# Performance work log

Hardware: AMD Instinct MI355X
Metric: run time of the kernel (lower is better)

## Reference

```python
import jax, jax.numpy as jnp
import numpy as np

HEADS = 12
IDX = 0


def setup_inputs() -> dict:
    key = jax.random.key(0)
    ks = jax.random.split(key, 6)
    B, H, W, C = 16, 64, 64, 384
    x = jax.random.normal(ks[0], (B, H * W, C), dtype=jnp.float32)
    qkv_w = jax.random.normal(ks[1], (3 * C, C), dtype=jnp.float32) * 0.02
    proj_w = jax.random.normal(ks[2], (C, C), dtype=jnp.float32) * 0.02
    proj_b = jax.random.normal(ks[3], (C,), dtype=jnp.float32) * 0.02
    lepe_w = jax.random.normal(ks[4], (C, 1, 3, 3), dtype=jnp.float32) * 0.02  # depthwise, torch OIHW with I=1
    lepe_b = jax.random.normal(ks[5], (C,), dtype=jnp.float32) * 0.02
    return {"x": x, "qkv_w": qkv_w, "proj_w": proj_w, "proj_b": proj_b,
            "lepe_w": lepe_w, "lepe_b": lepe_b, "H": H, "W": W}


def _lepe_forward(x, qkv_w, proj_w, proj_b, lepe_w, lepe_b, H, W):
    B, N, C = x.shape
    hd = C // HEADS
    scale = hd ** (-0.5)
    x_img = x.reshape(B, H, W, C)

    if IDX == 0:
        # vertical strips: attend over H within each column
        x_split = jnp.transpose(x_img, (0, 2, 1, 3)).reshape(B * W, H, C)
    else:
        x_split = x_img.reshape(B * H, W, C)
    S, L, _ = x_split.shape

    qkv = (x_split @ qkv_w.T).reshape(S, L, 3, HEADS, hd)
    qkv = jnp.transpose(qkv, (2, 0, 3, 1, 4))  # (3, S, heads, L, hd)
    q, k, v = qkv[0], qkv[1], qkv[2]

    attn = jnp.einsum('shld,shmd->shlm', q, k) * scale
    attn = jax.nn.softmax(attn, axis=-1)
    out = jnp.einsum('shlm,shmd->shld', attn, v)           # (S, heads, L, hd)
    out = jnp.transpose(out, (0, 2, 1, 3)).reshape(S, L, C)
    # faithful to torch: view(B, out_H, out_W, C).view(B, H*W, C) -- no permute back for idx==0
    out_flat = out.reshape(B, H * W, C)

    # depthwise 3x3 conv LePE on the original (H, W) layout
    lepe = jax.lax.conv_general_dilated(
        jnp.transpose(x_img, (0, 3, 1, 2)), lepe_w,
        window_strides=(1, 1), padding='SAME',
        feature_group_count=C,
        dimension_numbers=('NCHW', 'OIHW', 'NCHW'))
    lepe = lepe + lepe_b[None, :, None, None]
    lepe = jnp.transpose(lepe, (0, 2, 3, 1)).reshape(B, H * W, C)

    return (out_flat + lepe) @ proj_w.T + proj_b


def reference(x, qkv_w, proj_w, proj_b, lepe_w, lepe_b, H, W):
    return _lepe_forward(x, qkv_w, proj_w, proj_b, lepe_w, lepe_b, H, W)
```

## Files before the change

### kernel.cpp

```cpp
#include <hip/hip_runtime.h>


typedef _Float16 f16;
typedef _Float16 f16x8 __attribute__((ext_vector_type(8)));
typedef float    f32x4 __attribute__((ext_vector_type(4)));

__device__ __forceinline__ f32x4 mfma_16x16x32(f16x8 a, f16x8 b, f32x4 c) {
  return __builtin_amdgcn_mfma_f32_16x16x32_f16(a, b, c, 0, 0, 0);
}

__global__ __launch_bounds__(256) void k_cvt(const float* __restrict__ src,
                                             f16* __restrict__ dst, int n8) {
  int i = blockIdx.x * 256 + threadIdx.x;
  if (i >= n8) return;
  const f32x4* s4 = (const f32x4*)src;
  f32x4 a = s4[2 * i], b = s4[2 * i + 1];
  f16x8 o;
#pragma unroll
  for (int j = 0; j < 4; ++j) { o[j] = (f16)a[j]; o[4 + j] = (f16)b[j]; }
  *(f16x8*)&dst[(long)i * 8] = o;
}

template <int NDIM, bool FINAL>
__global__ __launch_bounds__(256) void k_gemm(const f16* __restrict__ A,
                                              const f16* __restrict__ Bt,
                                              const float* __restrict__ bias,
                                              f16* __restrict__ Ch,
                                              float* __restrict__ Cf) {
  constexpr int KD = 384;
  constexpr int LDSP = 72;
  constexpr int NT = NDIM / 128;
  __shared__ f16 As[128 * LDSP];
  __shared__ f16 Bs[128 * LDSP];

  const int tid = threadIdx.x;
  const int lane = tid & 63;
  const int wave = tid >> 6;
  const int wr = wave >> 1, wc = wave & 1;
  const int ln = lane & 15, quad = lane >> 4;
  const int q8 = quad * 8;
  const int mt = blockIdx.x / NT;
  const int nt = blockIdx.x % NT;
  const long m0 = (long)mt * 128;
  const int n0 = nt * 128;

  f32x4 acc[4][4] = {};

  for (int k0 = 0; k0 < KD; k0 += 64) {
#pragma unroll
    for (int r = 0; r < 4; ++r) {
      int flat = r * 256 + tid;
      int row = flat >> 3;
      int kk = (flat & 7) * 8;
      f16x8 av = *(const f16x8*)&A[(m0 + row) * KD + k0 + kk];
      *(f16x8*)&As[row * LDSP + kk] = av;
      f16x8 bv = *(const f16x8*)&Bt[(long)(n0 + row) * KD + k0 + kk];
      *(f16x8*)&Bs[row * LDSP + kk] = bv;
    }
    __syncthreads();
#pragma unroll
    for (int ks = 0; ks < 2; ++ks) {
      f16x8 a[4], b[4];
#pragma unroll
      for (int i = 0; i < 4; ++i)
        a[i] = *(const f16x8*)&As[(wr * 64 + i * 16 + ln) * LDSP + ks * 32 + q8];
#pragma unroll
      for (int j = 0; j < 4; ++j)
        b[j] = *(const f16x8*)&Bs[(wc * 64 + j * 16 + ln) * LDSP + ks * 32 + q8];
#pragma unroll
      for (int i = 0; i < 4; ++i)
#pragma unroll
        for (int j = 0; j < 4; ++j)
          acc[i][j] = mfma_16x16x32(a[i], b[j], acc[i][j]);
    }
    __syncthreads();
  }

#pragma unroll
  for (int i = 0; i < 4; ++i) {
#pragma unroll
    for (int j = 0; j < 4; ++j) {
      int gc = n0 + wc * 64 + j * 16 + ln;
#pragma unroll
      for (int r = 0; r < 4; ++r) {
        long gr = m0 + wr * 64 + i * 16 + quad * 4 + r;
        float v = acc[i][j][r];
        if (FINAL)
          Cf[gr * NDIM + gc] = v + bias[gc];
        else
          Ch[gr * (long)NDIM + gc] = (f16)v;
      }
    }
  }
}

__global__ __launch_bounds__(256) void k_lepe(const f16* __restrict__ x16,
                                              const float* __restrict__ lw,
                                              const float* __restrict__ lb,
                                              f16* __restrict__ afused) {
  __shared__ float ws[384 * 9];
  __shared__ float bs[384];
  for (int i = threadIdx.x; i < 384 * 9; i += 256) ws[i] = lw[i];
  for (int i = threadIdx.x; i < 384; i += 256) bs[i] = lb[i];
  __syncthreads();

  int chunk = blockIdx.x * 256 + threadIdx.x;
  int token = chunk / 48;
  int c0 = (chunk % 48) * 8;
  int b = token >> 12, n = token & 4095;
  int h = n >> 6, w = n & 63;

  float acc[8];
#pragma unroll
  for (int cc = 0; cc < 8; ++cc) acc[cc] = bs[c0 + cc];
#pragma unroll
  for (int ky = 0; ky < 3; ++ky) {
    int hh = h + ky - 1;
    if (hh < 0 || hh > 63) continue;
#pragma unroll
    for (int kx = 0; kx < 3; ++kx) {
      int ww = w + kx - 1;
      if (ww < 0 || ww > 63) continue;
      f16x8 xv = *(const f16x8*)&x16[((long)((b << 12) + (hh << 6) + ww)) * 384 + c0];
#pragma unroll
      for (int cc = 0; cc < 8; ++cc)
        acc[cc] += (float)xv[cc] * ws[(c0 + cc) * 9 + ky * 3 + kx];
    }
  }
  f16x8 o;
#pragma unroll
  for (int cc = 0; cc < 8; ++cc) o[cc] = (f16)acc[cc];
  *(f16x8*)&afused[(long)token * 384 + c0] = o;
}

__global__ __launch_bounds__(64) void k_attn(const f16* __restrict__ qkv,
                                             f16* __restrict__ afused) {
  __shared__ f16 vt[32 * 72];
  __shared__ f16 qkbuf[2 * 64 * 56];
  f16* qs = qkbuf;
  f16* ks = qkbuf + 64 * 56;
  f16* ps = qkbuf;

  const int lane = threadIdx.x;
  const int hh = blockIdx.x % 12;
  const int s = blockIdx.x / 12;
  const int b = s >> 6, w = s & 63;
  const int ln = lane & 15, quad = lane >> 4;
  const int q8 = quad * 8;
  const long baseTok = ((long)b << 12) + w;

#pragma unroll
  for (int r = 0; r < 4; ++r) {
    int flat = r * 64 + lane;
    int l = flat >> 2;
    int dg = (flat & 3) * 8;
    long ta = (baseTok + (long)l * 64) * 1152 + hh * 32 + dg;
    f16x8 qv = *(const f16x8*)&qkv[ta];
    f16x8 kv = *(const f16x8*)&qkv[ta + 384];
    f16x8 vv = *(const f16x8*)&qkv[ta + 768];
    *(f16x8*)&qs[l * 56 + dg] = qv;
    *(f16x8*)&ks[l * 56 + dg] = kv;
#pragma unroll
    for (int ii = 0; ii < 8; ++ii) vt[(dg + ii) * 72 + l] = vv[ii];
  }
  __syncthreads();

  f16x8 aq[4], bk[4];
#pragma unroll
  for (int i = 0; i < 4; ++i) aq[i] = *(const f16x8*)&qs[(i * 16 + ln) * 56 + q8];
#pragma unroll
  for (int j = 0; j < 4; ++j) bk[j] = *(const f16x8*)&ks[(j * 16 + ln) * 56 + q8];
  f32x4 sc[4][4] = {};
#pragma unroll
  for (int i = 0; i < 4; ++i)
#pragma unroll
    for (int j = 0; j < 4; ++j) sc[i][j] = mfma_16x16x32(aq[i], bk[j], sc[i][j]);
  __syncthreads();

  const float scale = 0.17677669529663687f;
  float rs[4][4];
#pragma unroll
  for (int i = 0; i < 4; ++i) {
#pragma unroll
    for (int r = 0; r < 4; ++r) {
      float m = -1e30f;
#pragma unroll
      for (int j = 0; j < 4; ++j) m = fmaxf(m, sc[i][j][r]);
#pragma unroll
      for (int off = 1; off < 16; off <<= 1) m = fmaxf(m, __shfl_xor(m, off, 64));
      m *= scale;
      float sum = 0.f;
#pragma unroll
      for (int j = 0; j < 4; ++j) {
        float p = __expf(sc[i][j][r] * scale - m);
        sc[i][j][r] = p;
        sum += p;
      }
#pragma unroll
      for (int off = 1; off < 16; off <<= 1) sum += __shfl_xor(sum, off, 64);
      rs[i][r] = 1.0f / sum;
    }
  }

#pragma unroll
  for (int i = 0; i < 4; ++i)
#pragma unroll
    for (int j = 0; j < 4; ++j)
#pragma unroll
      for (int r = 0; r < 4; ++r)
        ps[(i * 16 + quad * 4 + r) * 72 + j * 16 + ln] = (f16)sc[i][j][r];
  __syncthreads();

  f32x4 oc[4][2] = {};
#pragma unroll
  for (int ks2 = 0; ks2 < 2; ++ks2) {
    f16x8 ap[4], bv[2];
#pragma unroll
    for (int i = 0; i < 4; ++i)
      ap[i] = *(const f16x8*)&ps[(i * 16 + ln) * 72 + ks2 * 32 + q8];
#pragma unroll
    for (int j = 0; j < 2; ++j)
      bv[j] = *(const f16x8*)&vt[(j * 16 + ln) * 72 + ks2 * 32 + q8];
#pragma unroll
    for (int i = 0; i < 4; ++i)
#pragma unroll
      for (int j = 0; j < 2; ++j) oc[i][j] = mfma_16x16x32(ap[i], bv[j], oc[i][j]);
  }

#pragma unroll
  for (int i = 0; i < 4; ++i)
#pragma unroll
    for (int j = 0; j < 2; ++j)
#pragma unroll
      for (int r = 0; r < 4; ++r) {
        int l = i * 16 + quad * 4 + r;
        int d = j * 16 + ln;
        long g = ((long)b * 4096 + w * 64 + l) * 384 + hh * 32 + d;
        float v = oc[i][j][r] * rs[i][r];
        afused[g] = (f16)(v + (float)afused[g]);
      }
}

extern "C" void kernel_launch(void* const* d_in, const int* in_sizes, int n_in,
                              void* d_out, int out_size, void* d_ws, size_t ws_size,
                              hipStream_t stream) {
  const float* x      = (const float*)d_in[0];
  const float* qkv_w  = (const float*)d_in[1];
  const float* proj_w = (const float*)d_in[2];
  const float* proj_b = (const float*)d_in[3];
  const float* lepe_w = (const float*)d_in[4];
  const float* lepe_b = (const float*)d_in[5];
  float* out = (float*)d_out;

  char* ws = (char*)d_ws;
  f16* x16    = (f16*)(ws + 0);
  f16* w16    = (f16*)(ws + 50331648);
  f16* pw16   = (f16*)(ws + 51216384);
  f16* qkv16  = (f16*)(ws + 51511296);
  f16* afused = (f16*)(ws + 202506240);

  k_cvt<<<12288, 256, 0, stream>>>(x, x16, 3145728);
  k_cvt<<<216, 256, 0, stream>>>(qkv_w, w16, 55296);
  k_cvt<<<72, 256, 0, stream>>>(proj_w, pw16, 18432);
  k_gemm<1152, false><<<512 * 9, 256, 0, stream>>>(x16, w16, nullptr, qkv16, nullptr);
  k_lepe<<<12288, 256, 0, stream>>>(x16, lepe_w, lepe_b, afused);
  k_attn<<<1024 * 12, 64, 0, stream>>>(qkv16, afused);
  k_gemm<384, true><<<512 * 3, 256, 0, stream>>>(afused, pw16, proj_b, nullptr, out);
}
```

Measured before the change: 508.0 us.

## Fuse conversion into LePE, async LDS GEMM loads, restructure attention and proj fusion

```diff
diff --git a/kernel.cpp b/kernel.cpp
--- a/kernel.cpp
+++ b/kernel.cpp
@@ -7,6 +7,11 @@
 
 __device__ __forceinline__ f32x4 mfma_16x16x32(f16x8 a, f16x8 b, f32x4 c) {
   return __builtin_amdgcn_mfma_f32_16x16x32_f16(a, b, c, 0, 0, 0);
+}
+
+__device__ __forceinline__ void gl_lds16(const f16* g, f16* l) {
+  __builtin_amdgcn_global_load_lds((const __attribute__((address_space(1))) void*)g,
+                                   (__attribute__((address_space(3))) void*)l, 16, 0, 0);
 }
 
 __global__ __launch_bounds__(256) void k_cvt(const float* __restrict__ src,
@@ -21,83 +26,11 @@
   *(f16x8*)&dst[(long)i * 8] = o;
 }
 
-template <int NDIM, bool FINAL>
-__global__ __launch_bounds__(256) void k_gemm(const f16* __restrict__ A,
-                                              const f16* __restrict__ Bt,
-                                              const float* __restrict__ bias,
-                                              f16* __restrict__ Ch,
-                                              float* __restrict__ Cf) {
-  constexpr int KD = 384;
-  constexpr int LDSP = 72;
-  constexpr int NT = NDIM / 128;
-  __shared__ f16 As[128 * LDSP];
-  __shared__ f16 Bs[128 * LDSP];
-
-  const int tid = threadIdx.x;
-  const int lane = tid & 63;
-  const int wave = tid >> 6;
-  const int wr = wave >> 1, wc = wave & 1;
-  const int ln = lane & 15, quad = lane >> 4;
-  const int q8 = quad * 8;
-  const int mt = blockIdx.x / NT;
-  const int nt = blockIdx.x % NT;
-  const long m0 = (long)mt * 128;
-  const int n0 = nt * 128;
-
-  f32x4 acc[4][4] = {};
-
-  for (int k0 = 0; k0 < KD; k0 += 64) {
-#pragma unroll
-    for (int r = 0; r < 4; ++r) {
-      int flat = r * 256 + tid;
-      int row = flat >> 3;
-      int kk = (flat & 7) * 8;
-      f16x8 av = *(const f16x8*)&A[(m0 + row) * KD + k0 + kk];
-      *(f16x8*)&As[row * LDSP + kk] = av;
-      f16x8 bv = *(const f16x8*)&Bt[(long)(n0 + row) * KD + k0 + kk];
-      *(f16x8*)&Bs[row * LDSP + kk] = bv;
-    }
-    __syncthreads();
-#pragma unroll
-    for (int ks = 0; ks < 2; ++ks) {
-      f16x8 a[4], b[4];
-#pragma unroll
-      for (int i = 0; i < 4; ++i)
-        a[i] = *(const f16x8*)&As[(wr * 64 + i * 16 + ln) * LDSP + ks * 32 + q8];
-#pragma unroll
-      for (int j = 0; j < 4; ++j)
-        b[j] = *(const f16x8*)&Bs[(wc * 64 + j * 16 + ln) * LDSP + ks * 32 + q8];
-#pragma unroll
-      for (int i = 0; i < 4; ++i)
-#pragma unroll
-        for (int j = 0; j < 4; ++j)
-          acc[i][j] = mfma_16x16x32(a[i], b[j], acc[i][j]);
-    }
-    __syncthreads();
-  }
-
-#pragma unroll
-  for (int i = 0; i < 4; ++i) {
-#pragma unroll
-    for (int j = 0; j < 4; ++j) {
-      int gc = n0 + wc * 64 + j * 16 + ln;
-#pragma unroll
-      for (int r = 0; r < 4; ++r) {
-        long gr = m0 + wr * 64 + i * 16 + quad * 4 + r;
-        float v = acc[i][j][r];
-        if (FINAL)
-          Cf[gr * NDIM + gc] = v + bias[gc];
-        else
-          Ch[gr * (long)NDIM + gc] = (f16)v;
-      }
-    }
-  }
-}
-
-__global__ __launch_bounds__(256) void k_lepe(const f16* __restrict__ x16,
+__global__ __launch_bounds__(256) void k_prep(const float* __restrict__ x,
                                               const float* __restrict__ lw,
                                               const float* __restrict__ lb,
-                                              f16* __restrict__ afused) {
+                                              f16* __restrict__ x16,
+                                              f16* __restrict__ lepe16) {
   __shared__ float ws[384 * 9];
   __shared__ float bs[384];
   for (int i = threadIdx.x; i < 384 * 9; i += 256) ws[i] = lw[i];
@@ -106,13 +39,14 @@
 
   int chunk = blockIdx.x * 256 + threadIdx.x;
   int token = chunk / 48;
-  int c0 = (chunk % 48) * 8;
-  int b = token >> 12, n = token & 4095;
-  int h = n >> 6, w = n & 63;
-
-  float acc[8];
-#pragma unroll
-  for (int cc = 0; cc < 8; ++cc) acc[cc] = bs[c0 + cc];
+  int c0 = (chunk - token * 48) * 8;
+  int b = token >> 12, n = token & 4095, h = n >> 6, w = n & 63;
+  const float* xb = x + (long)(b << 12) * 384;
+
+  float a8[8];
+#pragma unroll
+  for (int cc = 0; cc < 8; ++cc) a8[cc] = bs[c0 + cc];
+  f16x8 cv;
 #pragma unroll
   for (int ky = 0; ky < 3; ++ky) {
     int hh = h + ky - 1;
@@ -121,131 +55,269 @@
     for (int kx = 0; kx < 3; ++kx) {
       int ww = w + kx - 1;
       if (ww < 0 || ww > 63) continue;
-      f16x8 xv = *(const f16x8*)&x16[((long)((b << 12) + (hh << 6) + ww)) * 384 + c0];
+      const float* p = xb + (long)((hh << 6) + ww) * 384 + c0;
+      float4 u = *(const float4*)p;
+      float4 v = *(const float4*)(p + 4);
+      float xs[8] = {u.x, u.y, u.z, u.w, v.x, v.y, v.z, v.w};
+      if (ky == 1 && kx == 1) {
+#pragma unroll
+        for (int cc = 0; cc < 8; ++cc) cv[cc] = (f16)xs[cc];
+      }
 #pragma unroll
       for (int cc = 0; cc < 8; ++cc)
-        acc[cc] += (float)xv[cc] * ws[(c0 + cc) * 9 + ky * 3 + kx];
+        a8[cc] += xs[cc] * ws[(c0 + cc) * 9 + ky * 3 + kx];
     }
   }
   f16x8 o;
 #pragma unroll
-  for (int cc = 0; cc < 8; ++cc) o[cc] = (f16)acc[cc];
-  *(f16x8*)&afused[(long)token * 384 + c0] = o;
-}
-
-__global__ __launch_bounds__(64) void k_attn(const f16* __restrict__ qkv,
-                                             f16* __restrict__ afused) {
-  __shared__ f16 vt[32 * 72];
-  __shared__ f16 qkbuf[2 * 64 * 56];
-  f16* qs = qkbuf;
-  f16* ks = qkbuf + 64 * 56;
-  f16* ps = qkbuf;
-
-  const int lane = threadIdx.x;
-  const int hh = blockIdx.x % 12;
-  const int s = blockIdx.x / 12;
-  const int b = s >> 6, w = s & 63;
-  const int ln = lane & 15, quad = lane >> 4;
-  const int q8 = quad * 8;
-  const long baseTok = ((long)b << 12) + w;
-
-#pragma unroll
-  for (int r = 0; r < 4; ++r) {
-    int flat = r * 64 + lane;
-    int l = flat >> 2;
-    int dg = (flat & 3) * 8;
-    long ta = (baseTok + (long)l * 64) * 1152 + hh * 32 + dg;
-    f16x8 qv = *(const f16x8*)&qkv[ta];
-    f16x8 kv = *(const f16x8*)&qkv[ta + 384];
-    f16x8 vv = *(const f16x8*)&qkv[ta + 768];
-    *(f16x8*)&qs[l * 56 + dg] = qv;
-    *(f16x8*)&ks[l * 56 + dg] = kv;
-#pragma unroll
-    for (int ii = 0; ii < 8; ++ii) vt[(dg + ii) * 72 + l] = vv[ii];
+  for (int cc = 0; cc < 8; ++cc) o[cc] = (f16)a8[cc];
+  *(f16x8*)&x16[(long)token * 384 + c0] = cv;
+  *(f16x8*)&lepe16[(long)token * 384 + c0] = o;
+}
+
+__global__ __launch_bounds__(256) void k_qkv(const f16* __restrict__ A,
+                                             const f16* __restrict__ Bt,
+                                             f16* __restrict__ C) {
+  __shared__ alignas(16) f16 As[128 * 64];
+  __shared__ alignas(16) f16 Bs[128 * 64];
+  const int tid = threadIdx.x;
+  const int lane = tid & 63;
+  const int wave = tid >> 6;
+  const int wr = wave >> 1, wc = wave & 1;
+  const int ln = lane & 15, quad = lane >> 4, q8 = quad * 8;
+  const int mt = blockIdx.x & 511;
+  const int nt = blockIdx.x >> 9;
+  const long m0 = (long)mt * 128;
+  const int n0 = nt * 128;
+
+  f32x4 acc[4][4] = {};
+  for (int k0 = 0; k0 < 384; k0 += 64) {
+#pragma unroll
+    for (int r = 0; r < 4; ++r) {
+      int flat = r * 256 + tid;
+      int row = flat >> 3, c8 = flat & 7;
+      int sc8 = (c8 ^ (row & 7)) * 8;
+      gl_lds16(&A[(m0 + row) * 384 + k0 + sc8], &As[flat * 8]);
+      gl_lds16(&Bt[(long)(n0 + row) * 384 + k0 + sc8], &Bs[flat * 8]);
+    }
+    __syncthreads();
+#pragma unroll
+    for (int ks = 0; ks < 2; ++ks) {
+      f16x8 a[4], b[4];
+#pragma unroll
+      for (int i = 0; i < 4; ++i)
+        a[i] = *(const f16x8*)&As[(wr * 64 + i * 16 + ln) * 64 +
+                                  ((ks * 4 + quad) ^ (ln & 7)) * 8];
+#pragma unroll
+      for (int j = 0; j < 4; ++j)
+        b[j] = *(const f16x8*)&Bs[(wc * 64 + j * 16 + ln) * 64 +
+                                  ((ks * 4 + quad) ^ (ln & 7)) * 8];
+#pragma unroll
+      for (int i = 0; i < 4; ++i)
+#pragma unroll
+        for (int j = 0; j < 4; ++j)
+          acc[i][j] = mfma_16x16x32(a[i], b[j], acc[i][j]);
+    }
+    __syncthreads();
   }
-  __syncthreads();
-
-  f16x8 aq[4], bk[4];
-#pragma unroll
-  for (int i = 0; i < 4; ++i) aq[i] = *(const f16x8*)&qs[(i * 16 + ln) * 56 + q8];
-#pragma unroll
-  for (int j = 0; j < 4; ++j) bk[j] = *(const f16x8*)&ks[(j * 16 + ln) * 56 + q8];
-  f32x4 sc[4][4] = {};
+
 #pragma unroll
   for (int i = 0; i < 4; ++i)
 #pragma unroll
-    for (int j = 0; j < 4; ++j) sc[i][j] = mfma_16x16x32(aq[i], bk[j], sc[i][j]);
-  __syncthreads();
-
-  const float scale = 0.17677669529663687f;
-  float rs[4][4];
-#pragma unroll
-  for (int i = 0; i < 4; ++i) {
+    for (int j = 0; j < 4; ++j) {
+      int gc = n0 + wc * 64 + j * 16 + ln;
+#pragma unroll
+      for (int r = 0; r < 4; ++r) {
+        int t = (int)m0 + wr * 64 + i * 16 + quad * 4 + r;
+        int nn = t & 4095;
+        long prow = (long)(t & ~4095) + ((nn & 63) << 6) + (nn >> 6);
+        C[prow * 1152 + gc] = (f16)acc[i][j][r];
+      }
+    }
+}
+
+__global__ __launch_bounds__(256) void k_attn(const f16* __restrict__ qkv,
+                                              f16* __restrict__ attnout) {
+  __shared__ alignas(16) f16 shp[4][7424];
+  const int lane = threadIdx.x & 63;
+  const int wave = threadIdx.x >> 6;
+  const int ln = lane & 15, quad = lane >> 4, q8 = quad * 8;
+  const int b = blockIdx.x >> 6, w = blockIdx.x & 63;
+  const long sbase = (long)b * 4096 + (long)w * 64;
+
+  f16* qs = shp[wave];
+  f16* ks = shp[wave] + 2560;
+  f16* vt = shp[wave] + 5120;
+  f16* ps = shp[wave];
+  f16* obuf = shp[wave];
+  const float qscale = 0.17677669529663687f;
+
+  for (int hi = 0; hi < 3; ++hi) {
+    const int hh = wave * 3 + hi;
 #pragma unroll
     for (int r = 0; r < 4; ++r) {
-      float m = -1e30f;
-#pragma unroll
-      for (int j = 0; j < 4; ++j) m = fmaxf(m, sc[i][j][r]);
-#pragma unroll
-      for (int off = 1; off < 16; off <<= 1) m = fmaxf(m, __shfl_xor(m, off, 64));
-      m *= scale;
-      float sum = 0.f;
-#pragma unroll
-      for (int j = 0; j < 4; ++j) {
-        float p = __expf(sc[i][j][r] * scale - m);
-        sc[i][j][r] = p;
-        sum += p;
-      }
-#pragma unroll
-      for (int off = 1; off < 16; off <<= 1) sum += __shfl_xor(sum, off, 64);
-      rs[i][r] = 1.0f / sum;
+      int flat = r * 64 + lane;
+      int l = flat >> 2, dg = (flat & 3) * 8;
+      long ta = (sbase + l) * 1152 + hh * 32 + dg;
+      f16x8 qv = *(const f16x8*)&qkv[ta];
+      f16x8 kv = *(const f16x8*)&qkv[ta + 384];
+      f16x8 vv = *(const f16x8*)&qkv[ta + 768];
+#pragma unroll
+      for (int ii = 0; ii < 8; ++ii) qv[ii] = (f16)((float)qv[ii] * qscale);
+      *(f16x8*)&qs[l * 40 + dg] = qv;
+      *(f16x8*)&ks[l * 40 + dg] = kv;
+#pragma unroll
+      for (int ii = 0; ii < 8; ++ii) vt[(dg + ii) * 72 + l] = vv[ii];
+    }
+    f16x8 aq[4], bk[4];
+#pragma unroll
+    for (int i = 0; i < 4; ++i) aq[i] = *(const f16x8*)&qs[(i * 16 + ln) * 40 + q8];
+#pragma unroll
+    for (int j = 0; j < 4; ++j) bk[j] = *(const f16x8*)&ks[(j * 16 + ln) * 40 + q8];
+    f32x4 sc[4][4] = {};
+#pragma unroll
+    for (int i = 0; i < 4; ++i)
+#pragma unroll
+      for (int j = 0; j < 4; ++j) sc[i][j] = mfma_16x16x32(aq[i], bk[j], sc[i][j]);
+
+    float rs[4][4];
+#pragma unroll
+    for (int i = 0; i < 4; ++i)
+#pragma unroll
+      for (int r = 0; r < 4; ++r) {
+        float m = -1e30f;
+#pragma unroll
+        for (int j = 0; j < 4; ++j) m = fmaxf(m, sc[i][j][r]);
+#pragma unroll
+        for (int off = 1; off < 16; off <<= 1) m = fmaxf(m, __shfl_xor(m, off, 64));
+        float sum = 0.f;
+#pragma unroll
+        for (int j = 0; j < 4; ++j) {
+          float p = __expf(sc[i][j][r] - m);
+          sc[i][j][r] = p;
+          sum += p;
+        }
+#pragma unroll
+        for (int off = 1; off < 16; off <<= 1) sum += __shfl_xor(sum, off, 64);
+        rs[i][r] = 1.0f / sum;
+      }
+
+#pragma unroll
+    for (int i = 0; i < 4; ++i)
+#pragma unroll
+      for (int j = 0; j < 4; ++j)
+#pragma unroll
+        for (int r = 0; r < 4; ++r)
+          ps[(i * 16 + quad * 4 + r) * 72 + j * 16 + ln] = (f16)sc[i][j][r];
+
+    f32x4 oc[4][2] = {};
+#pragma unroll
+    for (int k2 = 0; k2 < 2; ++k2) {
+      f16x8 ap[4], bv[2];
+#pragma unroll
+      for (int i = 0; i < 4; ++i)
+        ap[i] = *(const f16x8*)&ps[(i * 16 + ln) * 72 + k2 * 32 + q8];
+#pragma unroll
+      for (int j = 0; j < 2; ++j)
+        bv[j] = *(const f16x8*)&vt[(j * 16 + ln) * 72 + k2 * 32 + q8];
+#pragma unroll
+      for (int i = 0; i < 4; ++i)
+#pragma unroll
+        for (int j = 0; j < 2; ++j) oc[i][j] = mfma_16x16x32(ap[i], bv[j], oc[i][j]);
+    }
+
+#pragma unroll
+    for (int i = 0; i < 4; ++i)
+#pragma unroll
+      for (int j = 0; j < 2; ++j)
+#pragma unroll
+        for (int r = 0; r < 4; ++r)
+          obuf[(i * 16 + quad * 4 + r) * 40 + j * 16 + ln] =
+              (f16)(oc[i][j][r] * rs[i][r]);
+    {
+      int row = lane >> 1, hf = lane & 1;
+#pragma unroll
+      for (int rr = 0; rr < 2; ++rr) {
+        int rw = rr * 32 + row;
+        const f16* ob = &obuf[rw * 40 + hf * 16];
+        f16x8 o0 = *(const f16x8*)ob;
+        f16x8 o1 = *(const f16x8*)(ob + 8);
+        f16* gp = attnout + (sbase + rw) * 384 + hh * 32 + hf * 16;
+        *(f16x8*)gp = o0;
+        *(f16x8*)(gp + 8) = o1;
+      }
     }
   }
+}
+
+__global__ __launch_bounds__(256) void k_proj(const f16* __restrict__ A1,
+                                              const f16* __restrict__ A2,
+                                              const f16* __restrict__ Bt,
+                                              const float* __restrict__ bias,
+                                              float* __restrict__ Cf) {
+  __shared__ alignas(16) f16 As[128 * 64];
+  __shared__ alignas(16) f16 Bs[128 * 64];
+  const int tid = threadIdx.x;
+  const int lane = tid & 63;
+  const int wave = tid >> 6;
+  const int wr = wave >> 1, wc = wave & 1;
+  const int ln = lane & 15, quad = lane >> 4, q8 = quad * 8;
+  const int mt = blockIdx.x & 511;
+  const int nt = blockIdx.x >> 9;
+  const long m0 = (long)mt * 128;
+  const int n0 = nt * 128;
+
+  f32x4 acc[4][4] = {};
+  for (int k0 = 0; k0 < 384; k0 += 64) {
+#pragma unroll
+    for (int r = 0; r < 4; ++r) {
+      int flat = r * 256 + tid;
+      int row = flat >> 3, c8 = flat & 7;
+      int sc8 = (c8 ^ (row & 7)) * 8;
+      long ai = (m0 + row) * 384 + k0 + sc8;
+      f16x8 s = *(const f16x8*)&A1[ai] + *(const f16x8*)&A2[ai];
+      *(f16x8*)&As[flat * 8] = s;
+      gl_lds16(&Bt[(long)(n0 + row) * 384 + k0 + sc8], &Bs[flat * 8]);
+    }
+    __syncthreads();
+#pragma unroll
+    for (int ks = 0; ks < 2; ++ks) {
+      f16x8 a[4], b[4];
+#pragma unroll
+      for (int i = 0; i < 4; ++i)
+        a[i] = *(const f16x8*)&As[(wr * 64 + i * 16 + ln) * 64 +
+                                  ((ks * 4 + quad) ^ (ln & 7)) * 8];
+#pragma unroll
+      for (int j = 0; j < 4; ++j)
+        b[j] = *(const f16x8*)&Bs[(wc * 64 + j * 16 + ln) * 64 +
+                                  ((ks * 4 + quad) ^ (ln & 7)) * 8];
+#pragma unroll
+      for (int i = 0; i < 4; ++i)
+#pragma unroll
+        for (int j = 0; j < 4; ++j)
+          acc[i][j] = mfma_16x16x32(a[i], b[j], acc[i][j]);
+    }
+    __syncthreads();
+  }
 
 #pragma unroll
   for (int i = 0; i < 4; ++i)
 #pragma unroll
-    for (int j = 0; j < 4; ++j)
-#pragma unroll
-      for (int r = 0; r < 4; ++r)
-        ps[(i * 16 + quad * 4 + r) * 72 + j * 16 + ln] = (f16)sc[i][j][r];
-  __syncthreads();
-
-  f32x4 oc[4][2] = {};
-#pragma unroll
-  for (int ks2 = 0; ks2 < 2; ++ks2) {
-    f16x8 ap[4], bv[2];
-#pragma unroll
-    for (int i = 0; i < 4; ++i)
-      ap[i] = *(const f16x8*)&ps[(i * 16 + ln) * 72 + ks2 * 32 + q8];
-#pragma unroll
-    for (int j = 0; j < 2; ++j)
-      bv[j] = *(const f16x8*)&vt[(j * 16 + ln) * 72 + ks2 * 32 + q8];
-#pragma unroll
-    for (int i = 0; i < 4; ++i)
-#pragma unroll
-      for (int j = 0; j < 2; ++j) oc[i][j] = mfma_16x16x32(ap[i], bv[j], oc[i][j]);
-  }
-
-#pragma unroll
-  for (int i = 0; i < 4; ++i)
-#pragma unroll
-    for (int j = 0; j < 2; ++j)
+    for (int j = 0; j < 4; ++j) {
+      int gc = n0 + wc * 64 + j * 16 + ln;
 #pragma unroll
       for (int r = 0; r < 4; ++r) {
-        int l = i * 16 + quad * 4 + r;
-        int d = j * 16 + ln;
-        long g = ((long)b * 4096 + w * 64 + l) * 384 + hh * 32 + d;
-        float v = oc[i][j][r] * rs[i][r];
-        afused[g] = (f16)(v + (float)afused[g]);
-      }
+        long gr = m0 + wr * 64 + i * 16 + quad * 4 + r;
+        Cf[gr * 384 + gc] = acc[i][j][r] + bias[gc];
+      }
+    }
 }
 
 extern "C" void kernel_launch(void* const* d_in, const int* in_sizes, int n_in,
                               void* d_out, int out_size, void* d_ws, size_t ws_size,
                               hipStream_t stream) {
-  const float* x      = (const float*)d_in[0];
-  const float* qkv_w  = (const float*)d_in[1];
+  const float* x = (const float*)d_in[0];
+  const float* qkv_w = (const float*)d_in[1];
   const float* proj_w = (const float*)d_in[2];
   const float* proj_b = (const float*)d_in[3];
   const float* lepe_w = (const float*)d_in[4];
@@ -253,17 +325,17 @@
   float* out = (float*)d_out;
 
   char* ws = (char*)d_ws;
-  f16* x16    = (f16*)(ws + 0);
-  f16* w16    = (f16*)(ws + 50331648);
-  f16* pw16   = (f16*)(ws + 51216384);
-  f16* qkv16  = (f16*)(ws + 51511296);
-  f16* afused = (f16*)(ws + 202506240);
-
-  k_cvt<<<12288, 256, 0, stream>>>(x, x16, 3145728);
+  f16* w16 = (f16*)(ws + 0);
+  f16* pw16 = (f16*)(ws + 884736);
+  f16* x16 = (f16*)(ws + 1179648);
+  f16* attnout = x16;
+  f16* lepe16 = (f16*)(ws + 51511296);
+  f16* qkv16 = (f16*)(ws + 101842944);
+
   k_cvt<<<216, 256, 0, stream>>>(qkv_w, w16, 55296);
   k_cvt<<<72, 256, 0, stream>>>(proj_w, pw16, 18432);
-  k_gemm<1152, false><<<512 * 9, 256, 0, stream>>>(x16, w16, nullptr, qkv16, nullptr);
-  k_lepe<<<12288, 256, 0, stream>>>(x16, lepe_w, lepe_b, afused);
-  k_attn<<<1024 * 12, 64, 0, stream>>>(qkv16, afused);
-  k_gemm<384, true><<<512 * 3, 256, 0, stream>>>(afused, pw16, proj_b, nullptr, out);
-}
+  k_prep<<<12288, 256, 0, stream>>>(x, lepe_w, lepe_b, x16, lepe16);
+  k_qkv<<<512 * 9, 256, 0, stream>>>(x16, w16, qkv16);
+  k_attn<<<1024, 256, 0, stream>>>(qkv16, attnout);
+  k_proj<<<512 * 3, 256, 0, stream>>>(attnout, lepe16, pw16, proj_b, out);
+}
```

Result: faster. 491.8 us (-3.2%).
